# Kernel optimization log

Hardware: AMD Instinct MI355X
Metric: run time of the kernel (lower is better)

## Reference

```python
import jax, jax.numpy as jnp
import numpy as np

TEMPERATURE = 0.07
EPS = 1e-8  # torch CosineSimilarity eps default


def setup_inputs() -> dict:
    key = jax.random.key(0)
    k1, k2 = jax.random.split(key)
    N, D = 8192, 1024
    image_features = jax.random.normal(k1, (N, D), dtype=jnp.float32)
    text_features = jax.random.normal(k2, (N, D), dtype=jnp.float32)
    return {"image_features": image_features, "text_features": text_features}


def _normalize(x):
    # matches torch cosine similarity denominator clamp: norm >= eps
    n = jnp.sqrt(jnp.sum(x * x, axis=-1, keepdims=True))
    return x / jnp.maximum(n, EPS)


def reference(image_features, text_features):
    # cosine similarity via normalize + GEMM (same math as broadcasted NxNxD form)
    img_n = _normalize(image_features)  # [N, D]
    txt_n = _normalize(text_features)   # [N, D]
    logits = jnp.einsum('id,jd->ij', img_n, txt_n) / TEMPERATURE  # [N, N]

    N = logits.shape[0]
    labels = jnp.arange(N)
    # cross-entropy with labels = diagonal indices
    logp_i2t = jax.nn.log_softmax(logits, axis=-1)      # rows: image -> text
    logp_t2i = jax.nn.log_softmax(logits.T, axis=-1)    # rows: text -> image
    loss_i2t = -jnp.mean(logp_i2t[labels, labels])
    loss_t2i = -jnp.mean(logp_t2i[labels, labels])
    return (loss_i2t + loss_t2i) / 2
```

## Files before the change

### kernel.cpp

```cpp
#include <hip/hip_runtime.h>


#define BM 256
#define BN 256
#define BKB 128

typedef float floatx4 __attribute__((ext_vector_type(4)));
typedef int   intx4   __attribute__((ext_vector_type(4)));
typedef int   intx8   __attribute__((ext_vector_type(8)));

__device__ __forceinline__ void gload_lds16(const unsigned char* g, unsigned char* lds) {
    __builtin_amdgcn_global_load_lds(
        (const __attribute__((address_space(1))) void*)g,
        (__attribute__((address_space(3))) void*)lds,
        16, 0, 0);
}

__global__ __launch_bounds__(256)
void normalize_fp8(const float* __restrict__ img, const float* __restrict__ txt,
                   unsigned int* __restrict__ oimg, unsigned int* __restrict__ otxt,
                   float* __restrict__ sums, float* __restrict__ out, int N) {
    const int gi = blockIdx.x * 256 + threadIdx.x;
    if (gi < 2 * N) sums[gi] = 0.f;
    if (gi == 0) out[0] = 0.f;

    const int gw = blockIdx.x * 4 + (threadIdx.x >> 6);
    const int lane = threadIdx.x & 63;
    const float* in = (gw < N) ? img : txt;
    unsigned int* o = (gw < N) ? oimg : otxt;
    const int row = (gw < N) ? gw : gw - N;
    const float4* rp = (const float4*)(in + (size_t)row * 1024);

    float4 v[4];
    float ss = 0.f;
    #pragma unroll
    for (int j = 0; j < 4; ++j) {
        v[j] = rp[j * 64 + lane];
        ss += v[j].x * v[j].x + v[j].y * v[j].y + v[j].z * v[j].z + v[j].w * v[j].w;
    }
    #pragma unroll
    for (int o2 = 1; o2 < 64; o2 <<= 1) ss += __shfl_xor(ss, o2);
    const float inv = 16.0f / fmaxf(sqrtf(ss), 1e-8f);
    #pragma unroll
    for (int j = 0; j < 4; ++j) {
        int p = __builtin_amdgcn_cvt_pk_fp8_f32(v[j].x * inv, v[j].y * inv, 0, false);
        p = __builtin_amdgcn_cvt_pk_fp8_f32(v[j].z * inv, v[j].w * inv, p, true);
        const int d = j * 64 + lane;
        const int c = (d >> 2) & 7;
        const int pp = (c & 1) * 4 + (c >> 1);
        const int dp = (d & ~31) | (pp * 4 + (d & 3));
        o[(size_t)row * 256 + dp] = (unsigned int)p;
    }
}

__global__ __launch_bounds__(512, 2)
void gemm_exp_kernel(const unsigned char* __restrict__ A,
                     const unsigned char* __restrict__ B,
                     float* __restrict__ rowsum, float* __restrict__ colsum,
                     float* __restrict__ diag, int K, float scale) {
    const int id = blockIdx.x;
    const int idp = id >> 3;
    const int bm = (id & 7) * 4 + (idp & 3);
    const int bn = idp >> 2;

    __shared__ unsigned char As[2 * 2 * 256 * 64];
    __shared__ unsigned char Bs[2 * 2 * 256 * 64];

    const int tid = threadIdx.x;
    const int lane = tid & 63;
    const int wave = tid >> 6;
    const int quad = lane >> 4;
    const int lanelo = lane & 15;
    const int wr = wave >> 2;
    const int wc = wave & 3;
    const int wrow = wr * 128;
    const int wcol = wc * 64;

    floatx4 acc[8][4] = {};

    const int c0 = tid;
    const int c1 = tid + 512;
    const int r0 = c0 >> 2, r1 = c1 >> 2;
    const int kg0 = ((c0 & 3) ^ ((r0 >> 1) & 3)) * 16;
    const int kg1 = ((c1 & 3) ^ ((r1 >> 1) & 3)) * 16;

    const unsigned char* pa0 = A + ((size_t)bm * BM + r0) * K + kg0;
    const unsigned char* pa1 = A + ((size_t)bm * BM + r1) * K + kg1;
    const unsigned char* pb0 = B + ((size_t)bn * BN + r0) * K + kg0;
    const unsigned char* pb1 = B + ((size_t)bn * BN + r1) * K + kg1;

    const int swx = (quad ^ ((lanelo >> 1) & 3)) * 16;
    const int aoffB = (wrow + lanelo) * 64 + swx;
    const int boffB = (wcol + lanelo) * 64 + swx;

    auto stage = [&](int k, int buf) {
        unsigned char* dA = As + buf * 32768 + c0 * 16;
        unsigned char* dB = Bs + buf * 32768 + c0 * 16;
        #pragma unroll
        for (int w = 0; w < 2; ++w) {
            gload_lds16(pa0 + k + w * 64, dA + w * 16384);
            gload_lds16(pa1 + k + w * 64, dA + 8192 + w * 16384);
            gload_lds16(pb0 + k + w * 64, dB + w * 16384);
            gload_lds16(pb1 + k + w * 64, dB + 8192 + w * 16384);
        }
    };

    stage(0, 0);
    stage(BKB, 1);
    for (int k = 0, it = 0; k < K; k += BKB, ++it) {
        const int buf = it & 1;
        if (k + BKB < K) { asm volatile("s_waitcnt vmcnt(8)" ::: "memory"); }
        else             { asm volatile("s_waitcnt vmcnt(0)" ::: "memory"); }
        __builtin_amdgcn_s_barrier();

        const unsigned char* Ab = As + buf * 32768;
        const unsigned char* Bb = Bs + buf * 32768;

        intx8 bg[4];
        #pragma unroll
        for (int t = 0; t < 4; ++t) {
            const intx4 blo = *(const intx4*)(Bb + boffB + t * 1024);
            const intx4 bhi = *(const intx4*)(Bb + 16384 + boffB + t * 1024);
            bg[t] = __builtin_shufflevector(blo, bhi, 0, 1, 2, 3, 4, 5, 6, 7);
        }

        #pragma unroll
        for (int ph = 0; ph < 4; ++ph) {
            intx8 af[2];
            #pragma unroll
            for (int t = 0; t < 2; ++t) {
                const int tm = ph * 2 + t;
                const intx4 alo = *(const intx4*)(Ab + aoffB + tm * 1024);
                const intx4 ahi = *(const intx4*)(Ab + 16384 + aoffB + tm * 1024);
                af[t] = __builtin_shufflevector(alo, ahi, 0, 1, 2, 3, 4, 5, 6, 7);
            }
            __builtin_amdgcn_s_setprio(1);
            #pragma unroll
            for (int t = 0; t < 2; ++t)
                #pragma unroll
                for (int tn = 0; tn < 4; ++tn)
                    acc[ph * 2 + t][tn] = __builtin_amdgcn_mfma_scale_f32_16x16x128_f8f6f4(
                        af[t], bg[tn], acc[ph * 2 + t][tn],
                        0, 0,
                        0, 127,
                        0, 127);
            __builtin_amdgcn_s_setprio(0);
        }

        __builtin_amdgcn_s_barrier();
        if (k + 2 * BKB < K) stage(k + 2 * BKB, buf);
    }

    const int growb = bm * BM + wrow;
    const int gcolb = bn * BN + wcol;

    #pragma unroll
    for (int tm = 0; tm < 8; ++tm)
        #pragma unroll
        for (int tn = 0; tn < 4; ++tn)
            #pragma unroll
            for (int r = 0; r < 4; ++r) {
                const float l = acc[tm][tn][r] * scale;
                const int grow = growb + tm * 16 + quad * 4 + r;
                const int gcol = gcolb + tn * 16 + lanelo;
                if (grow == gcol) diag[grow] = l;
                acc[tm][tn][r] = __expf(l);
            }

    #pragma unroll
    for (int tm = 0; tm < 8; ++tm) {
        floatx4 rs = acc[tm][0] + acc[tm][1] + acc[tm][2] + acc[tm][3];
        #pragma unroll
        for (int r = 0; r < 4; ++r) {
            float v = rs[r];
            v += __shfl_xor(v, 1);
            v += __shfl_xor(v, 2);
            v += __shfl_xor(v, 4);
            v += __shfl_xor(v, 8);
            if (lanelo == 0)
                atomicAdd(&rowsum[growb + tm * 16 + quad * 4 + r], v);
        }
    }

    #pragma unroll
    for (int tn = 0; tn < 4; ++tn) {
        float cs = 0.f;
        #pragma unroll
        for (int tm = 0; tm < 8; ++tm)
            cs += acc[tm][tn][0] + acc[tm][tn][1] + acc[tm][tn][2] + acc[tm][tn][3];
        cs += __shfl_xor(cs, 16);
        cs += __shfl_xor(cs, 32);
        if (quad == 0)
            atomicAdd(&colsum[gcolb + tn * 16 + lanelo], cs);
    }
}

__global__ __launch_bounds__(256)
void final_reduce(const float* __restrict__ rowsum, const float* __restrict__ colsum,
                  const float* __restrict__ diag, float* __restrict__ out, int n) {
    const int i = blockIdx.x * 256 + threadIdx.x;
    const int t = threadIdx.x;
    float v = 0.5f * (logf(rowsum[i]) + logf(colsum[i])) - diag[i];
    #pragma unroll
    for (int o = 1; o < 64; o <<= 1) v += __shfl_xor(v, o);
    __shared__ float ws[4];
    if ((t & 63) == 0) ws[t >> 6] = v;
    __syncthreads();
    if (t == 0) atomicAdd(out, (ws[0] + ws[1] + ws[2] + ws[3]) / (float)n);
}

extern "C" void kernel_launch(void* const* d_in, const int* in_sizes, int n_in,
                              void* d_out, int out_size, void* d_ws, size_t ws_size,
                              hipStream_t stream) {
    const float* img = (const float*)d_in[0];
    const float* txt = (const float*)d_in[1];
    float* out = (float*)d_out;

    const int D = 1024;
    const int N = in_sizes[0] / D;

    unsigned char* imgq = (unsigned char*)d_ws;
    unsigned char* txtq = imgq + (size_t)N * D;
    float* rowsum = (float*)(txtq + (size_t)N * D);
    float* colsum = rowsum + N;
    float* diag = colsum + N;

    normalize_fp8<<<2 * N / 4, 256, 0, stream>>>(img, txt, (unsigned int*)imgq,
                                                 (unsigned int*)txtq, rowsum, out, N);

    gemm_exp_kernel<<<(N / BM) * (N / BN), 512, 0, stream>>>(
        imgq, txtq, rowsum, colsum, diag, D, 1.0f / (256.0f * 0.07f));
    final_reduce<<<N / 256, 256, 0, stream>>>(rowsum, colsum, diag, out, N);
}
```

Before: 184.8 us.

## Interleave global-to-LDS prefetch across MFMA phases with per-phase barriers

Rewrites the GEMM main loop so the next tiles' global-to-LDS loads are spread across the four MFMA phases instead of issued in one burst after the loop body. The A-tile load mapping is remapped so each wave loads row groups that can be issued incrementally, and the loop adds a barrier pair around every phase, similar to ping-pong style scheduling. The goal is to smooth memory traffic and overlap it with matrix math. The cost is many more barriers per iteration and more intricate vmcnt accounting that could stall or break correctness if the counts are off.

```diff
diff --git a/kernel.cpp b/kernel.cpp
--- a/kernel.cpp
+++ b/kernel.cpp
@@ -71,84 +71,110 @@
     const int wave = tid >> 6;
     const int quad = lane >> 4;
     const int lanelo = lane & 15;
-    const int wr = wave >> 2;
-    const int wc = wave & 3;
-    const int wrow = wr * 128;
-    const int wcol = wc * 64;
+    const int wrow = (wave >> 2) * 128;
+    const int wcol = (wave & 3) * 64;
 
     floatx4 acc[8][4] = {};
 
-    const int c0 = tid;
-    const int c1 = tid + 512;
-    const int r0 = c0 >> 2, r1 = c1 >> 2;
-    const int kg0 = ((c0 & 3) ^ ((r0 >> 1) & 3)) * 16;
-    const int kg1 = ((c1 & 3) ^ ((r1 >> 1) & 3)) * 16;
-
-    const unsigned char* pa0 = A + ((size_t)bm * BM + r0) * K + kg0;
-    const unsigned char* pa1 = A + ((size_t)bm * BM + r1) * K + kg1;
+    const int r0 = tid >> 2;
+    const int kg0 = ((tid & 3) ^ ((r0 >> 1) & 3)) * 16;
     const unsigned char* pb0 = B + ((size_t)bn * BN + r0) * K + kg0;
-    const unsigned char* pb1 = B + ((size_t)bn * BN + r1) * K + kg1;
+    const unsigned char* pb1 = pb0 + (size_t)128 * K;
+    unsigned char* ldsB = Bs + tid * 16;
+
+    const int wndA = wave >> 2;
+    const int rowOffA = (wave & 1) * 16 + ((wave & 2) ? 128 : 0) + (lane >> 2);
+    const int slotA = lane & 3;
+    const int kgA = ((slotA ^ ((rowOffA >> 1) & 3)) * 16) + wndA * 64;
+    const unsigned char* pa = A + ((size_t)bm * BM + rowOffA) * K + kgA;
+    unsigned char* ldsA = As + wndA * 16384 + rowOffA * 64 + slotA * 16;
 
     const int swx = (quad ^ ((lanelo >> 1) & 3)) * 16;
     const int aoffB = (wrow + lanelo) * 64 + swx;
     const int boffB = (wcol + lanelo) * 64 + swx;
 
-    auto stage = [&](int k, int buf) {
-        unsigned char* dA = As + buf * 32768 + c0 * 16;
-        unsigned char* dB = Bs + buf * 32768 + c0 * 16;
-        #pragma unroll
-        for (int w = 0; w < 2; ++w) {
-            gload_lds16(pa0 + k + w * 64, dA + w * 16384);
-            gload_lds16(pa1 + k + w * 64, dA + 8192 + w * 16384);
-            gload_lds16(pb0 + k + w * 64, dB + w * 16384);
-            gload_lds16(pb1 + k + w * 64, dB + 8192 + w * 16384);
-        }
-    };
-
-    stage(0, 0);
-    stage(BKB, 1);
-    for (int k = 0, it = 0; k < K; k += BKB, ++it) {
-        const int buf = it & 1;
-        if (k + BKB < K) { asm volatile("s_waitcnt vmcnt(8)" ::: "memory"); }
-        else             { asm volatile("s_waitcnt vmcnt(0)" ::: "memory"); }
-        __builtin_amdgcn_s_barrier();
-
+    const int NT = K >> 7;
+
+    #pragma unroll
+    for (int t = 0; t < 2; ++t) {
+        const int k = t * BKB;
+        const int bo = t * 32768;
+        gload_lds16(pb0 + k,      ldsB + bo);
+        gload_lds16(pb0 + k + 64, ldsB + bo + 16384);
+        gload_lds16(pb1 + k,      ldsB + bo + 8192);
+        gload_lds16(pb1 + k + 64, ldsB + bo + 8192 + 16384);
+        #pragma unroll
+        for (int j = 0; j < 4; ++j)
+            gload_lds16(pa + (size_t)(j * 32) * K + k, ldsA + bo + j * 2048);
+    }
+    asm volatile("s_waitcnt vmcnt(8)" ::: "memory");
+    __builtin_amdgcn_s_barrier();
+
+    for (int t = 0; t < NT; ++t) {
+        const int buf = t & 1;
         const unsigned char* Ab = As + buf * 32768;
         const unsigned char* Bb = Bs + buf * 32768;
+        const int bo2 = buf * 32768;
+        const int bo1 = (buf ^ 1) * 32768;
+        const int k1 = (t + 1) * BKB;
+        const int k2 = (t + 2) * BKB;
 
         intx8 bg[4];
         #pragma unroll
-        for (int t = 0; t < 4; ++t) {
-            const intx4 blo = *(const intx4*)(Bb + boffB + t * 1024);
-            const intx4 bhi = *(const intx4*)(Bb + 16384 + boffB + t * 1024);
-            bg[t] = __builtin_shufflevector(blo, bhi, 0, 1, 2, 3, 4, 5, 6, 7);
-        }
-
-        #pragma unroll
-        for (int ph = 0; ph < 4; ++ph) {
+        for (int p = 0; p < 4; ++p) {
+            if (p == 0) {
+                #pragma unroll
+                for (int tn = 0; tn < 4; ++tn) {
+                    const intx4 blo = *(const intx4*)(Bb + boffB + tn * 1024);
+                    const intx4 bhi = *(const intx4*)(Bb + 16384 + boffB + tn * 1024);
+                    bg[tn] = __builtin_shufflevector(blo, bhi, 0, 1, 2, 3, 4, 5, 6, 7);
+                }
+            }
             intx8 af[2];
             #pragma unroll
-            for (int t = 0; t < 2; ++t) {
-                const int tm = ph * 2 + t;
+            for (int u = 0; u < 2; ++u) {
+                const int tm = p * 2 + u;
                 const intx4 alo = *(const intx4*)(Ab + aoffB + tm * 1024);
                 const intx4 ahi = *(const intx4*)(Ab + 16384 + aoffB + tm * 1024);
-                af[t] = __builtin_shufflevector(alo, ahi, 0, 1, 2, 3, 4, 5, 6, 7);
-            }
+                af[u] = __builtin_shufflevector(alo, ahi, 0, 1, 2, 3, 4, 5, 6, 7);
+            }
+
+            if (p == 0) {
+                if (t >= 1 && t + 1 < NT)
+                    gload_lds16(pa + (size_t)(3 * 32) * K + k1, ldsA + bo1 + 3 * 2048);
+            } else if (p == 1) {
+                if (t + 2 < NT) {
+                    gload_lds16(pb0 + k2,      ldsB + bo2);
+                    gload_lds16(pb0 + k2 + 64, ldsB + bo2 + 16384);
+                    gload_lds16(pb1 + k2,      ldsB + bo2 + 8192);
+                    gload_lds16(pb1 + k2 + 64, ldsB + bo2 + 8192 + 16384);
+                    gload_lds16(pa + k2,       ldsA + bo2);
+                }
+            } else if (p == 2) {
+                if (t + 2 < NT)
+                    gload_lds16(pa + (size_t)(1 * 32) * K + k2, ldsA + bo2 + 1 * 2048);
+            } else {
+                if (t + 2 < NT)
+                    gload_lds16(pa + (size_t)(2 * 32) * K + k2, ldsA + bo2 + 2 * 2048);
+                if (t < NT - 2)       { asm volatile("s_waitcnt vmcnt(7)" ::: "memory"); }
+                else if (t == NT - 2) { asm volatile("s_waitcnt vmcnt(0)" ::: "memory"); }
+            }
+
+            __builtin_amdgcn_s_barrier();
+            asm volatile("s_waitcnt lgkmcnt(0)" ::: "memory");
             __builtin_amdgcn_s_setprio(1);
             #pragma unroll
-            for (int t = 0; t < 2; ++t)
+            for (int u = 0; u < 2; ++u)
                 #pragma unroll
                 for (int tn = 0; tn < 4; ++tn)
-                    acc[ph * 2 + t][tn] = __builtin_amdgcn_mfma_scale_f32_16x16x128_f8f6f4(
-                        af[t], bg[tn], acc[ph * 2 + t][tn],
+                    acc[p * 2 + u][tn] = __builtin_amdgcn_mfma_scale_f32_16x16x128_f8f6f4(
+                        af[u], bg[tn], acc[p * 2 + u][tn],
                         0, 0,
                         0, 127,
                         0, 127);
             __builtin_amdgcn_s_setprio(0);
+            __builtin_amdgcn_s_barrier();
         }
-
-        __builtin_amdgcn_s_barrier();
-        if (k + 2 * BKB < K) stage(k + 2 * BKB, buf);
     }
 
     const int growb = bm * BM + wrow;
```

Result: slower. 195.1 us (+5.6%).
